# Performance work log

Hardware: AMD Instinct MI355X
Metric: run time of the kernel (lower is better)

Reference implementation:

```python
import jax, jax.numpy as jnp
import numpy as np

BS = 16  # block_size

def setup_inputs() -> dict:
    key = jax.random.key(0)
    k1, k2, k3, k4, k5 = jax.random.split(key, 5)
    B, C, H, W = 4, 192, 256, 256
    x = jax.random.normal(k1, (B, C, H, W), dtype=jnp.float32)
    s = 1.0 / np.sqrt(C)
    qkv_w = jax.random.normal(k2, (3 * C, C), dtype=jnp.float32) * s
    qkv_b = jax.random.normal(k3, (3 * C,), dtype=jnp.float32) * 0.01
    proj_w = jax.random.normal(k4, (C, C), dtype=jnp.float32) * s
    proj_b = jax.random.normal(k5, (C,), dtype=jnp.float32) * 0.01
    return {"x": x, "qkv_w": qkv_w, "qkv_b": qkv_b, "proj_w": proj_w, "proj_b": proj_b}

def reference(x, qkv_w, qkv_b, proj_w, proj_b):
    B, C, H, W = x.shape
    nh, nw = H // BS, W // BS
    N = BS * BS  # tokens per window
    # [B,C,H,W] -> [B*nh*nw, C, N]  (windowing, matches torch unfold/unfold)
    xb = x.reshape(B, C, nh, BS, nw, BS).transpose(0, 2, 4, 1, 3, 5)
    xb = xb.reshape(B * nh * nw, C, N)
    # 1x1-conv QKV projection as a GEMM over channels
    qkv = jnp.einsum('oc,bcn->bon', qkv_w, xb) + qkv_b[None, :, None]  # [Bb,3C,N]
    q, k, v = jnp.split(qkv, 3, axis=1)  # each [Bb, C, N]
    # attention: softmax(q^T k) over last dim (no scaling, as in original)
    att = jax.nn.softmax(jnp.einsum('bcn,bcm->bnm', q, k), axis=-1)  # [Bb,N,N]
    out = jnp.einsum('bnm,bcm->bcn', att, v)  # [Bb, C, N]
    # un-window back to [B, C, H, W]
    y = out.reshape(B, nh, nw, C, BS, BS).transpose(0, 3, 1, 4, 2, 5)
    y = y.reshape(B, C, H, W)
    # 1x1-conv output projection + residual
    proj = jnp.einsum('oc,bchw->bohw', proj_w, y) + proj_b[None, :, None, None]
    return proj + x
```

## Files before the change

kernel.cpp:

```cpp
#include <hip/hip_runtime.h>
#include <stdint.h>

typedef _Float16 f16;
typedef __attribute__((ext_vector_type(8))) _Float16 f16x8;
typedef __attribute__((ext_vector_type(4))) float f32x4;

#define MFMA(a, b, c) __builtin_amdgcn_mfma_f32_16x16x32_f16((a), (b), (c), 0, 0, 0)

static constexpr int C = 192;
static constexpr int N = 256;

__global__ void wconv_kernel(const float* __restrict__ qkv_w, const float* __restrict__ proj_w,
                             f16* __restrict__ wq, f16* __restrict__ wp) {
    int i = blockIdx.x * 256 + threadIdx.x;
    if (i < 576 * 192) wq[i] = (f16)qkv_w[i];
    if (i < 192 * 192) wp[i] = (f16)proj_w[i];
}

#define XS 200
__global__ __launch_bounds__(256, 4)
void qkv_kernel(const float* __restrict__ x, const f16* __restrict__ wq,
                const float* __restrict__ qkv_b,
                f16* __restrict__ qT, f16* __restrict__ kT, f16* __restrict__ vv) {
    __shared__ f16 xs[64 * XS];
    const int tid = threadIdx.x;
    const int wg = blockIdx.x;
    const int win = wg >> 2, tb = wg & 3;
    const int batch = win >> 8, wh = (win >> 4) & 15, ww = win & 15;
    const int i0 = tb * 4;

    for (int e = 0; e < 12; ++e) {
        int f = e * 1024 + tid * 4;
        int c = f >> 6, nl = f & 63;
        int i = nl >> 4, j = nl & 15;
        const float4 v4 = *(const float4*)(x + (((size_t)(batch * C + c) * 256 + (wh * 16 + i0 + i)) * 256 + ww * 16 + j));
        xs[(nl + 0) * XS + c] = (f16)v4.x;
        xs[(nl + 1) * XS + c] = (f16)v4.y;
        xs[(nl + 2) * XS + c] = (f16)v4.z;
        xs[(nl + 3) * XS + c] = (f16)v4.w;
    }
    __syncthreads();

    const int wave = tid >> 6, lane = tid & 63, l15 = lane & 15, qd = lane >> 4;
    for (int rb = wave; rb < 9; rb += 4) {
        f32x4 acc[4][4] = {};
#pragma unroll
        for (int k = 0; k < 6; ++k) {
            const int c0 = k * 32 + qd * 8;
            f16x8 af[4], bf[4];
#pragma unroll
            for (int mi = 0; mi < 4; ++mi)
                af[mi] = *(const f16x8*)(wq + (rb * 64 + mi * 16 + l15) * C + c0);
#pragma unroll
            for (int ti = 0; ti < 4; ++ti)
                bf[ti] = *(const f16x8*)(xs + (ti * 16 + l15) * XS + c0);
#pragma unroll
            for (int mi = 0; mi < 4; ++mi)
#pragma unroll
                for (int ti = 0; ti < 4; ++ti)
                    acc[mi][ti] = MFMA(af[mi], bf[ti], acc[mi][ti]);
        }
#pragma unroll
        for (int mi = 0; mi < 4; ++mi) {
            const int ob = rb * 64 + mi * 16 + qd * 4;
            const float b0 = qkv_b[ob + 0], b1 = qkv_b[ob + 1], b2 = qkv_b[ob + 2], b3 = qkv_b[ob + 3];
#pragma unroll
            for (int ti = 0; ti < 4; ++ti) {
                const int tok = tb * 64 + ti * 16 + l15;
                const size_t gt = (size_t)win * 256 + tok;
                if (ob < 384) {
                    union { f16 h[4]; uint2 u; } pk;
                    pk.h[0] = (f16)(acc[mi][ti][0] + b0);
                    pk.h[1] = (f16)(acc[mi][ti][1] + b1);
                    pk.h[2] = (f16)(acc[mi][ti][2] + b2);
                    pk.h[3] = (f16)(acc[mi][ti][3] + b3);
                    f16* dst = (ob < 192) ? (qT + gt * C + ob) : (kT + gt * C + (ob - 192));
                    *(uint2*)dst = pk.u;
                } else {
                    const int c2 = ob - 384;
                    vv[((size_t)win * C + c2 + 0) * 256 + tok] = (f16)(acc[mi][ti][0] + b0);
                    vv[((size_t)win * C + c2 + 1) * 256 + tok] = (f16)(acc[mi][ti][1] + b1);
                    vv[((size_t)win * C + c2 + 2) * 256 + tok] = (f16)(acc[mi][ti][2] + b2);
                    vv[((size_t)win * C + c2 + 3) * 256 + tok] = (f16)(acc[mi][ti][3] + b3);
                }
            }
        }
    }
}

#define SQS 200
#define SPS 264
__global__ __launch_bounds__(256, 4)
void attn_kernel(const f16* __restrict__ qT, const f16* __restrict__ kT,
                 const f16* __restrict__ vv, const f16* __restrict__ wp,
                 const float* __restrict__ proj_b, const float* __restrict__ x,
                 float* __restrict__ out) {
    __shared__ f16 sQ[64 * SQS];
    __shared__ f16 sP[64 * SPS];
    __shared__ float sRed[4][64];
    __shared__ float sMax[64];
    __shared__ float sSum[64];

    const int tid = threadIdx.x;
    const int wg = blockIdx.x;
    const int win = wg >> 2, rblk = wg & 3;
    const int n0 = rblk * 64;
    const int batch = win >> 8, wh = (win >> 4) & 15, ww = win & 15;
    const int wave = tid >> 6, lane = tid & 63, l15 = lane & 15, qd = lane >> 4;

    for (int it = 0; it < 6; ++it) {
        int ch = it * 256 + tid;
        int n = ch / 24, c8 = (ch % 24) * 8;
        *(f16x8*)(sQ + n * SQS + c8) = *(const f16x8*)(qT + ((size_t)win * 256 + n0 + n) * C + c8);
    }
    __syncthreads();

    f32x4 accS[4][4] = {};
#pragma unroll
    for (int k = 0; k < 6; ++k) {
        const int c0 = k * 32 + qd * 8;
        f16x8 af[4], bf[4];
#pragma unroll
        for (int mi = 0; mi < 4; ++mi)
            af[mi] = *(const f16x8*)(sQ + (mi * 16 + l15) * SQS + c0);
#pragma unroll
        for (int ti = 0; ti < 4; ++ti)
            bf[ti] = *(const f16x8*)(kT + ((size_t)win * 256 + wave * 64 + ti * 16 + l15) * C + c0);
#pragma unroll
        for (int mi = 0; mi < 4; ++mi)
#pragma unroll
            for (int ti = 0; ti < 4; ++ti)
                accS[mi][ti] = MFMA(af[mi], bf[ti], accS[mi][ti]);
    }

    float pm[4][4];
#pragma unroll
    for (int mi = 0; mi < 4; ++mi)
#pragma unroll
        for (int r = 0; r < 4; ++r) {
            float m = accS[mi][0][r];
            m = fmaxf(m, accS[mi][1][r]);
            m = fmaxf(m, accS[mi][2][r]);
            m = fmaxf(m, accS[mi][3][r]);
#pragma unroll
            for (int d = 1; d < 16; d <<= 1) m = fmaxf(m, __shfl_xor(m, d, 64));
            pm[mi][r] = m;
        }
    if (l15 == 0) {
#pragma unroll
        for (int mi = 0; mi < 4; ++mi)
#pragma unroll
            for (int r = 0; r < 4; ++r) sRed[wave][mi * 16 + qd * 4 + r] = pm[mi][r];
    }
    __syncthreads();
    if (tid < 64)
        sMax[tid] = fmaxf(fmaxf(sRed[0][tid], sRed[1][tid]), fmaxf(sRed[2][tid], sRed[3][tid]));
    __syncthreads();

    float ps[4][4];
#pragma unroll
    for (int mi = 0; mi < 4; ++mi)
#pragma unroll
        for (int r = 0; r < 4; ++r) {
            const float M = sMax[mi * 16 + qd * 4 + r];
            float s = 0.f;
#pragma unroll
            for (int ti = 0; ti < 4; ++ti) {
                float e = __expf(accS[mi][ti][r] - M);
                accS[mi][ti][r] = e;
                s += e;
            }
#pragma unroll
            for (int d = 1; d < 16; d <<= 1) s += __shfl_xor(s, d, 64);
            ps[mi][r] = s;
        }
    if (l15 == 0) {
#pragma unroll
        for (int mi = 0; mi < 4; ++mi)
#pragma unroll
            for (int r = 0; r < 4; ++r) sRed[wave][mi * 16 + qd * 4 + r] = ps[mi][r];
    }
    __syncthreads();
    if (tid < 64) sSum[tid] = sRed[0][tid] + sRed[1][tid] + sRed[2][tid] + sRed[3][tid];
#pragma unroll
    for (int mi = 0; mi < 4; ++mi)
#pragma unroll
        for (int ti = 0; ti < 4; ++ti)
#pragma unroll
            for (int r = 0; r < 4; ++r)
                sP[(mi * 16 + qd * 4 + r) * SPS + wave * 64 + ti * 16 + l15] = (f16)accS[mi][ti][r];
    __syncthreads();

    f32x4 accO[4][3] = {};
#pragma unroll
    for (int k = 0; k < 8; ++k) {
        const int m0 = k * 32 + qd * 8;
        f16x8 af[4], bf[3];
#pragma unroll
        for (int tn = 0; tn < 4; ++tn)
            af[tn] = *(const f16x8*)(sP + (tn * 16 + l15) * SPS + m0);
#pragma unroll
        for (int tc = 0; tc < 3; ++tc)
            bf[tc] = *(const f16x8*)(vv + ((size_t)win * C + wave * 48 + tc * 16 + l15) * 256 + m0);
#pragma unroll
        for (int tn = 0; tn < 4; ++tn)
#pragma unroll
            for (int tc = 0; tc < 3; ++tc)
                accO[tn][tc] = MFMA(af[tn], bf[tc], accO[tn][tc]);
    }
    f16* sOT = sQ;
#pragma unroll
    for (int tn = 0; tn < 4; ++tn)
#pragma unroll
        for (int r = 0; r < 4; ++r) {
            const int n = tn * 16 + qd * 4 + r;
            const float rs = 1.0f / sSum[n];
#pragma unroll
            for (int tc = 0; tc < 3; ++tc)
                sOT[n * SQS + wave * 48 + tc * 16 + l15] = (f16)(accO[tn][tc][r] * rs);
        }
    __syncthreads();

    f32x4 accP[3][4] = {};
#pragma unroll
    for (int k = 0; k < 6; ++k) {
        const int c0 = k * 32 + qd * 8;
        f16x8 af[3], bf[4];
#pragma unroll
        for (int to = 0; to < 3; ++to)
            af[to] = *(const f16x8*)(wp + (wave * 48 + to * 16 + l15) * C + c0);
#pragma unroll
        for (int tn = 0; tn < 4; ++tn)
            bf[tn] = *(const f16x8*)(sOT + (tn * 16 + l15) * SQS + c0);
#pragma unroll
        for (int to = 0; to < 3; ++to)
#pragma unroll
            for (int tn = 0; tn < 4; ++tn)
                accP[to][tn] = MFMA(af[to], bf[tn], accP[to][tn]);
    }
#pragma unroll
    for (int to = 0; to < 3; ++to)
#pragma unroll
        for (int r = 0; r < 4; ++r) {
            const int o = wave * 48 + to * 16 + qd * 4 + r;
            const float pb = proj_b[o];
#pragma unroll
            for (int tn = 0; tn < 4; ++tn) {
                const size_t idx = (((size_t)(batch * C + o) * 256) + wh * 16 + rblk * 4 + tn) * 256 + ww * 16 + l15;
                out[idx] = accP[to][tn][r] + pb + x[idx];
            }
        }
}

extern "C" void kernel_launch(void* const* d_in, const int* in_sizes, int n_in,
                              void* d_out, int out_size, void* d_ws, size_t ws_size,
                              hipStream_t stream) {
    const float* x      = (const float*)d_in[0];
    const float* qkv_w  = (const float*)d_in[1];
    const float* qkv_b  = (const float*)d_in[2];
    const float* proj_w = (const float*)d_in[3];
    const float* proj_b = (const float*)d_in[4];
    float* out = (float*)d_out;

    char* ws = (char*)d_ws;
    const size_t QKV_BYTES = (size_t)1024 * 256 * 192 * 2;
    f16* qT = (f16*)(ws);
    f16* kT = (f16*)(ws + QKV_BYTES);
    f16* vv = (f16*)(ws + 2 * QKV_BYTES);
    f16* wq = (f16*)(ws + 3 * QKV_BYTES);
    f16* wp = (f16*)(ws + 3 * QKV_BYTES + 576 * 192 * 2);

    wconv_kernel<<<432, 256, 0, stream>>>(qkv_w, proj_w, wq, wp);
    qkv_kernel<<<4096, 256, 0, stream>>>(x, wq, qkv_b, qT, kT, vv);
    attn_kernel<<<4096, 256, 0, stream>>>(qT, kT, vv, wp, proj_b, x, out);
}
```

Baseline: 786.2 us.

## Repack Q/K into channel-quad-major layout and halve P shared buffer

Q and K are now stored as [win][C/4][token][4] packs instead of token-major rows. The qkv kernel can then write them as contiguous 8-byte packs, and the attention kernel reads K fragments as two coalesced uint2 loads. The softmax probabilities are packed to fp16 in registers and staged through a half-width shared buffer in two phases with extra barriers. This cuts LDS use, and the launch bound changes to 3 blocks per SM. The block-to-window mapping is also permuted so that the groups of blocks sharing a window are spread differently. The extra syncs and split loads add overhead and may offset the gains.

```diff
diff --git a/kernel.cpp b/kernel.cpp
--- a/kernel.cpp
+++ b/kernel.cpp
@@ -8,7 +8,8 @@
 #define MFMA(a, b, c) __builtin_amdgcn_mfma_f32_16x16x32_f16((a), (b), (c), 0, 0, 0)
 
 static constexpr int C = 192;
-static constexpr int N = 256;
+
+union U8x { uint2 u2[2]; f16x8 v; };
 
 __global__ void wconv_kernel(const float* __restrict__ qkv_w, const float* __restrict__ proj_w,
                              f16* __restrict__ wq, f16* __restrict__ wp) {
@@ -21,7 +22,7 @@
 __global__ __launch_bounds__(256, 4)
 void qkv_kernel(const float* __restrict__ x, const f16* __restrict__ wq,
                 const float* __restrict__ qkv_b,
-                f16* __restrict__ qT, f16* __restrict__ kT, f16* __restrict__ vv) {
+                f16* __restrict__ Qp, f16* __restrict__ Kp, f16* __restrict__ vv) {
     __shared__ f16 xs[64 * XS];
     const int tid = threadIdx.x;
     const int wg = blockIdx.x;
@@ -67,15 +68,15 @@
 #pragma unroll
             for (int ti = 0; ti < 4; ++ti) {
                 const int tok = tb * 64 + ti * 16 + l15;
-                const size_t gt = (size_t)win * 256 + tok;
                 if (ob < 384) {
                     union { f16 h[4]; uint2 u; } pk;
                     pk.h[0] = (f16)(acc[mi][ti][0] + b0);
                     pk.h[1] = (f16)(acc[mi][ti][1] + b1);
                     pk.h[2] = (f16)(acc[mi][ti][2] + b2);
                     pk.h[3] = (f16)(acc[mi][ti][3] + b3);
-                    f16* dst = (ob < 192) ? (qT + gt * C + ob) : (kT + gt * C + (ob - 192));
-                    *(uint2*)dst = pk.u;
+                    const int c4 = (ob < 192) ? (ob >> 2) : ((ob - 192) >> 2);
+                    f16* base = (ob < 192) ? Qp : Kp;
+                    *(uint2*)(base + (((size_t)win * 48 + c4) * 256 + tok) * 4) = pk.u;
                 } else {
                     const int c2 = ob - 384;
                     vv[((size_t)win * C + c2 + 0) * 256 + tok] = (f16)(acc[mi][ti][0] + b0);
@@ -89,9 +90,9 @@
 }
 
 #define SQS 200
-#define SPS 264
-__global__ __launch_bounds__(256, 4)
-void attn_kernel(const f16* __restrict__ qT, const f16* __restrict__ kT,
+#define SPS 136
+__global__ __launch_bounds__(256, 3)
+void attn_kernel(const f16* __restrict__ Qp, const f16* __restrict__ Kp,
                  const f16* __restrict__ vv, const f16* __restrict__ wp,
                  const float* __restrict__ proj_b, const float* __restrict__ x,
                  float* __restrict__ out) {
@@ -103,15 +104,17 @@
 
     const int tid = threadIdx.x;
     const int wg = blockIdx.x;
-    const int win = wg >> 2, rblk = wg & 3;
+    const int win = ((wg >> 5) << 3) | (wg & 7);
+    const int rblk = (wg >> 3) & 3;
     const int n0 = rblk * 64;
     const int batch = win >> 8, wh = (win >> 4) & 15, ww = win & 15;
     const int wave = tid >> 6, lane = tid & 63, l15 = lane & 15, qd = lane >> 4;
 
-    for (int it = 0; it < 6; ++it) {
+    for (int it = 0; it < 12; ++it) {
         int ch = it * 256 + tid;
-        int n = ch / 24, c8 = (ch % 24) * 8;
-        *(f16x8*)(sQ + n * SQS + c8) = *(const f16x8*)(qT + ((size_t)win * 256 + n0 + n) * C + c8);
+        int n = ch & 63, c4 = ch >> 6;
+        *(uint2*)(sQ + n * SQS + c4 * 4) =
+            *(const uint2*)(Qp + (((size_t)win * 48 + c4) * 256 + n0 + n) * 4);
     }
     __syncthreads();
 
@@ -119,13 +122,20 @@
 #pragma unroll
     for (int k = 0; k < 6; ++k) {
         const int c0 = k * 32 + qd * 8;
+        const int c4 = c0 >> 2;
         f16x8 af[4], bf[4];
 #pragma unroll
         for (int mi = 0; mi < 4; ++mi)
             af[mi] = *(const f16x8*)(sQ + (mi * 16 + l15) * SQS + c0);
 #pragma unroll
-        for (int ti = 0; ti < 4; ++ti)
-            bf[ti] = *(const f16x8*)(kT + ((size_t)win * 256 + wave * 64 + ti * 16 + l15) * C + c0);
+        for (int ti = 0; ti < 4; ++ti) {
+            const int m = wave * 64 + ti * 16 + l15;
+            const size_t a = (((size_t)win * 48 + c4) * 256 + m) * 4;
+            U8x b;
+            b.u2[0] = *(const uint2*)(Kp + a);
+            b.u2[1] = *(const uint2*)(Kp + a + 1024);
+            bf[ti] = b.v;
+        }
 #pragma unroll
         for (int mi = 0; mi < 4; ++mi)
 #pragma unroll
@@ -138,10 +148,8 @@
     for (int mi = 0; mi < 4; ++mi)
 #pragma unroll
         for (int r = 0; r < 4; ++r) {
-            float m = accS[mi][0][r];
-            m = fmaxf(m, accS[mi][1][r]);
-            m = fmaxf(m, accS[mi][2][r]);
-            m = fmaxf(m, accS[mi][3][r]);
+            float m = fmaxf(fmaxf(accS[mi][0][r], accS[mi][1][r]),
+                            fmaxf(accS[mi][2][r], accS[mi][3][r]));
 #pragma unroll
             for (int d = 1; d < 16; d <<= 1) m = fmaxf(m, __shfl_xor(m, d, 64));
             pm[mi][r] = m;
@@ -157,6 +165,8 @@
         sMax[tid] = fmaxf(fmaxf(sRed[0][tid], sRed[1][tid]), fmaxf(sRed[2][tid], sRed[3][tid]));
     __syncthreads();
 
+    union PK { f16 h[4]; uint2 u; };
+    PK pH[4][4];
     float ps[4][4];
 #pragma unroll
     for (int mi = 0; mi < 4; ++mi)
@@ -167,7 +177,7 @@
 #pragma unroll
             for (int ti = 0; ti < 4; ++ti) {
                 float e = __expf(accS[mi][ti][r] - M);
-                accS[mi][ti][r] = e;
+                pH[mi][ti].h[r] = (f16)e;
                 s += e;
             }
 #pragma unroll
@@ -182,32 +192,41 @@
     }
     __syncthreads();
     if (tid < 64) sSum[tid] = sRed[0][tid] + sRed[1][tid] + sRed[2][tid] + sRed[3][tid];
-#pragma unroll
-    for (int mi = 0; mi < 4; ++mi)
-#pragma unroll
-        for (int ti = 0; ti < 4; ++ti)
-#pragma unroll
-            for (int r = 0; r < 4; ++r)
-                sP[(mi * 16 + qd * 4 + r) * SPS + wave * 64 + ti * 16 + l15] = (f16)accS[mi][ti][r];
-    __syncthreads();
 
     f32x4 accO[4][3] = {};
 #pragma unroll
-    for (int k = 0; k < 8; ++k) {
-        const int m0 = k * 32 + qd * 8;
-        f16x8 af[4], bf[3];
-#pragma unroll
-        for (int tn = 0; tn < 4; ++tn)
-            af[tn] = *(const f16x8*)(sP + (tn * 16 + l15) * SPS + m0);
-#pragma unroll
-        for (int tc = 0; tc < 3; ++tc)
-            bf[tc] = *(const f16x8*)(vv + ((size_t)win * C + wave * 48 + tc * 16 + l15) * 256 + m0);
-#pragma unroll
-        for (int tn = 0; tn < 4; ++tn)
+    for (int h = 0; h < 2; ++h) {
+        if ((wave >> 1) == h) {
+            const int cl = (wave & 1) * 64;
+#pragma unroll
+            for (int mi = 0; mi < 4; ++mi)
+#pragma unroll
+                for (int ti = 0; ti < 4; ++ti)
+#pragma unroll
+                    for (int r = 0; r < 4; ++r)
+                        sP[(mi * 16 + qd * 4 + r) * SPS + cl + ti * 16 + l15] = pH[mi][ti].h[r];
+        }
+        __syncthreads();
+#pragma unroll
+        for (int k = 0; k < 4; ++k) {
+            const int ml = k * 32 + qd * 8;
+            const int m0 = h * 128 + ml;
+            f16x8 af[4], bf[3];
+#pragma unroll
+            for (int tn = 0; tn < 4; ++tn)
+                af[tn] = *(const f16x8*)(sP + (tn * 16 + l15) * SPS + ml);
 #pragma unroll
             for (int tc = 0; tc < 3; ++tc)
-                accO[tn][tc] = MFMA(af[tn], bf[tc], accO[tn][tc]);
-    }
+                bf[tc] = *(const f16x8*)(vv + ((size_t)win * C + wave * 48 + tc * 16 + l15) * 256 + m0);
+#pragma unroll
+            for (int tn = 0; tn < 4; ++tn)
+#pragma unroll
+                for (int tc = 0; tc < 3; ++tc)
+                    accO[tn][tc] = MFMA(af[tn], bf[tc], accO[tn][tc]);
+        }
+        if (h == 0) __syncthreads();
+    }
+
     f16* sOT = sQ;
 #pragma unroll
     for (int tn = 0; tn < 4; ++tn)
@@ -264,13 +283,13 @@
 
     char* ws = (char*)d_ws;
     const size_t QKV_BYTES = (size_t)1024 * 256 * 192 * 2;
-    f16* qT = (f16*)(ws);
-    f16* kT = (f16*)(ws + QKV_BYTES);
+    f16* Qp = (f16*)(ws);
+    f16* Kp = (f16*)(ws + QKV_BYTES);
     f16* vv = (f16*)(ws + 2 * QKV_BYTES);
     f16* wq = (f16*)(ws + 3 * QKV_BYTES);
     f16* wp = (f16*)(ws + 3 * QKV_BYTES + 576 * 192 * 2);
 
     wconv_kernel<<<432, 256, 0, stream>>>(qkv_w, proj_w, wq, wp);
-    qkv_kernel<<<4096, 256, 0, stream>>>(x, wq, qkv_b, qT, kT, vv);
-    attn_kernel<<<4096, 256, 0, stream>>>(qT, kT, vv, wp, proj_b, x, out);
-}
+    qkv_kernel<<<4096, 256, 0, stream>>>(x, wq, qkv_b, Qp, Kp, vv);
+    attn_kernel<<<4096, 256, 0, stream>>>(Qp, Kp, vv, wp, proj_b, x, out);
+}
```

New measurement: 698.9 us. 1.12x faster.
